# Kernel optimization log

Measured on AMD Instinct MI355X. Metric: run time of the kernel, lower is better.

## Reference

```python
import jax, jax.numpy as jnp
import numpy as np

N, G, E = 100000, 32768, 1000000
F, H = 64, 64


def _mlp(x, w1, b1, w2, b2):
    # Linear -> SiLU -> Linear (matches nn.Sequential in the torch module)
    return jax.nn.silu(x @ w1 + b1) @ w2 + b2


def setup_inputs() -> dict:
    key = jax.random.key(0)
    ks = jax.random.split(key, 24)

    def lin(k, fan_in, fan_out):
        s = 1.0 / np.sqrt(fan_in)
        kw, kb = jax.random.split(k)
        w = jax.random.uniform(kw, (fan_in, fan_out), jnp.float32, -s, s)
        b = jax.random.uniform(kb, (fan_out,), jnp.float32, -s, s)
        return w, b

    node_w1, node_b1 = lin(ks[0], F, H)
    node_w2, node_b2 = lin(ks[1], H, H)
    edge_w1, edge_b1 = lin(ks[2], 6, H)
    edge_w2, edge_b2 = lin(ks[3], H, H)
    msg_w1, msg_b1 = lin(ks[4], 2 * H, H)
    msg_w2, msg_b2 = lin(ks[5], H, H)
    upd_w1, upd_b1 = lin(ks[6], H, H)
    upd_w2, upd_b2 = lin(ks[7], H, H)

    return {
        "node_features": jax.random.normal(ks[8], (N, F), jnp.float32),
        "node_pos": jax.random.normal(ks[9], (N, 3), jnp.float32),
        "grid_pos": jax.random.normal(ks[10], (G, 3), jnp.float32),
        "orientations": jax.random.normal(ks[11], (N, 3, 3), jnp.float32),
        "edge_index": jnp.stack([
            jax.random.randint(ks[12], (E,), 0, N),
            jax.random.randint(ks[13], (E,), 0, G),
        ]),
        "node_w1": node_w1, "node_b1": node_b1, "node_w2": node_w2, "node_b2": node_b2,
        "edge_w1": edge_w1, "edge_b1": edge_b1, "edge_w2": edge_w2, "edge_b2": edge_b2,
        "msg_w1": msg_w1, "msg_b1": msg_b1, "msg_w2": msg_w2, "msg_b2": msg_b2,
        "upd_w1": upd_w1, "upd_b1": upd_b1, "upd_w2": upd_w2, "upd_b2": upd_b2,
    }


def reference(node_features, node_pos, grid_pos, orientations, edge_index,
              node_w1, node_b1, node_w2, node_b2,
              edge_w1, edge_b1, edge_w2, edge_b2,
              msg_w1, msg_b1, msg_w2, msg_b2,
              upd_w1, upd_b1, upd_w2, upd_b2):
    source, target = edge_index[0], edge_index[1]
    num_grid = grid_pos.shape[0]

    # node MLP
    h_node = _mlp(node_features, node_w1, node_b1, node_w2, node_b2)  # [N,H]

    # per-edge message with orientation-aware projection
    pos_s = node_pos[source]                 # [E,3]
    rel = grid_pos[target] - pos_s           # [E,3]
    # bmm(rel[:,None,:], R[source]).squeeze(1) == einsum ei,eij->ej
    trel = jnp.einsum("ei,eij->ej", rel, orientations[source])
    edge_attr = jnp.concatenate([pos_s, trel], axis=-1)        # [E,6]
    e_feat = _mlp(edge_attr, edge_w1, edge_b1, edge_w2, edge_b2)
    msg_in = jnp.concatenate([h_node[source], e_feat], axis=-1)  # [E,2H]
    messages = _mlp(msg_in, msg_w1, msg_b1, msg_w2, msg_b2)      # [E,H]

    # scatter-mean into grid buckets (mask out-of-range targets)
    valid = (target >= 0) & (target < num_grid)
    idx = jnp.where(valid, target, 0)
    msg_masked = jnp.where(valid[:, None], messages, 0.0)
    sums = jax.ops.segment_sum(msg_masked, idx, num_segments=num_grid)
    cnts = jax.ops.segment_sum(valid.astype(jnp.float32), idx, num_segments=num_grid)
    grid_feat = sums / jnp.maximum(cnts, 1.0)[:, None]

    return _mlp(grid_feat, upd_w1, upd_b1, upd_w2, upd_b2)  # [G,H]
```

## Files before the change

### kernel.cpp

```cpp
#include <hip/hip_runtime.h>
#include <cstdint>

typedef __attribute__((ext_vector_type(8))) short short8;
typedef __attribute__((ext_vector_type(4))) float f32x4;
typedef unsigned short u16;

__device__ __forceinline__ float b2f(u16 u) {
  union { unsigned int i; float f; } v; v.i = ((unsigned int)u) << 16; return v.f;
}
__device__ __forceinline__ u16 f2b(float f) {
  union { float f; unsigned int i; } v; v.f = f;
  unsigned int x = v.i;
  return (u16)((x + 0x7fffu + ((x >> 16) & 1u)) >> 16);
}
__device__ __forceinline__ float silu_f(float x) { return x / (1.0f + __expf(-x)); }

__device__ __forceinline__ float loadF(const void* p, long i, int isf32) {
  if (isf32) return ((const float*)p)[i];
  return b2f(((const u16*)p)[i]);
}

struct Ptrs { const void* p[20]; int n[20]; };

#define FW_NW1 0
#define FW_NW2 4096
#define FW_UW1 8192
#define FW_UW2 12288
#define FW_EW1 16384
#define FW_NB1 16768
#define FW_NB2 16832
#define FW_UB1 16896
#define FW_UB2 16960
#define FW_EB1 17024
#define FW_EB2 17088
#define FW_MB1 17152
#define FW_MB2 17216
#define FW_TOTAL 17280

#define IMG_EW2 0
#define IMG_MW1 4608
#define IMG_MW2 13312
#define IMG_TOTAL 17920

__global__ __launch_bounds__(256) void detect_k(Ptrs a, int* flags) {
  int j = blockIdx.x;
  const u16* q = (const u16*)a.p[j];
  int n = a.n[j];
  int m = n < 4096 ? n : 4096;
  int cnt = 0;
  for (int i = threadIdx.x; i < m; i += 256) {
    unsigned e = (q[i] >> 7) & 0xffu;
    if (e >= 0xC0u) cnt++;
  }
  __shared__ int tot;
  if (threadIdx.x == 0) tot = 0;
  __syncthreads();
  if (cnt) atomicAdd(&tot, cnt);
  __syncthreads();
  if (threadIdx.x == 0) flags[j] = (tot >= 2) ? 1 : 0;
}

__global__ __launch_bounds__(256) void prep_k(Ptrs a, const int* flags,
                                              u16* img, float* fw) {
  int i = blockIdx.x * 256 + threadIdx.x;
  if (i < IMG_TOTAL) {
    u16 val = 0;
    if (i < IMG_MW1) {
      int nn = i / 72, k = i % 72;
      if (k < 64) val = f2b(loadF(a.p[10], (long)k * 64 + nn, flags[10]));
    } else if (i < IMG_MW2) {
      int t2 = i - IMG_MW1; int nn = t2 / 136, k = t2 % 136;
      if (k < 128) val = f2b(loadF(a.p[12], (long)k * 64 + nn, flags[12]));
    } else {
      int t2 = i - IMG_MW2; int nn = t2 / 72, k = t2 % 72;
      if (k < 64) val = f2b(loadF(a.p[14], (long)k * 64 + nn, flags[14]));
    }
    img[i] = val;
  } else if (i < IMG_TOTAL + FW_TOTAL) {
    int j = i - IMG_TOTAL;
    float v;
    if (j < 4096)            v = loadF(a.p[4],  j,          flags[4]);
    else if (j < 8192)       v = loadF(a.p[6],  j - 4096,   flags[6]);
    else if (j < 12288)      v = loadF(a.p[16], j - 8192,   flags[16]);
    else if (j < 16384)      v = loadF(a.p[18], j - 12288,  flags[18]);
    else if (j < 16768)      v = loadF(a.p[8],  j - 16384,  flags[8]);
    else {
      int b = j - 16768; int seg = b >> 6, c = b & 63;
      const void* bp; int bf;
      switch (seg) {
        case 0: bp = a.p[5];  bf = flags[5];  break;
        case 1: bp = a.p[7];  bf = flags[7];  break;
        case 2: bp = a.p[17]; bf = flags[17]; break;
        case 3: bp = a.p[19]; bf = flags[19]; break;
        case 4: bp = a.p[9];  bf = flags[9];  break;
        case 5: bp = a.p[11]; bf = flags[11]; break;
        case 6: bp = a.p[13]; bf = flags[13]; break;
        default: bp = a.p[15]; bf = flags[15]; break;
      }
      v = loadF(bp, c, bf);
    }
    fw[j] = v;
  }
}

__global__ __launch_bounds__(256) void hist_k(const int* __restrict__ eidx,
                                              int* __restrict__ cnt, long E, int G) {
  long i = (long)blockIdx.x * 256 + threadIdx.x;
  const long stride = (long)gridDim.x * 256;
  for (; i < E; i += stride) {
    int tg = eidx[E + i];
    if (tg >= 0 && tg < G) atomicAdd(&cnt[tg], 1);
  }
}

__global__ __launch_bounds__(1024) void scan_k(const int* __restrict__ cnt,
                                               int* __restrict__ cursor,
                                               int* __restrict__ evp, int G) {
  __shared__ int sd[1024];
  __shared__ int carry;
  const int t = threadIdx.x;
  if (t == 0) carry = 0;
  __syncthreads();
  for (int c0 = 0; c0 < G; c0 += 1024) {
    int i = c0 + t;
    int v = (i < G) ? cnt[i] : 0;
    sd[t] = v;
    __syncthreads();
    for (int off = 1; off < 1024; off <<= 1) {
      int x = (t >= off) ? sd[t - off] : 0;
      __syncthreads();
      sd[t] += x;
      __syncthreads();
    }
    int excl = sd[t] - v + carry;
    if (i < G) cursor[i] = excl;
    int tot = sd[1023];
    __syncthreads();
    if (t == 0) carry += tot;
    __syncthreads();
  }
  if (t == 0) *evp = carry;
}

__global__ __launch_bounds__(256) void scat_k(const int* __restrict__ eidx,
                                              int* __restrict__ cursor,
                                              unsigned int* __restrict__ pkS,
                                              long E, int G) {
  long i = (long)blockIdx.x * 256 + threadIdx.x;
  const long stride = (long)gridDim.x * 256;
  for (; i < E; i += stride) {
    int tg = eidx[E + i];
    if (tg >= 0 && tg < G) {
      int s = eidx[i];
      int p = atomicAdd(&cursor[tg], 1);
      pkS[p] = (unsigned int)s | ((unsigned int)tg << 17);
    }
  }
}

__global__ __launch_bounds__(256) void node_mlp(
    const void* x, const int* flags, const float* fw, u16* out, int nrows)
{
  __shared__ float xs[64][68];
  __shared__ float w1s[64][68];
  __shared__ float w2s[64][68];
  __shared__ float b1s[64];
  __shared__ float b2s[64];
  const int t = threadIdx.x;
  const int xf = flags[0];
  const long rbase = (long)blockIdx.x * 64;
  for (int i = t; i < 4096; i += 256) {
    int k = i >> 6, cc = i & 63;
    w1s[k][cc] = fw[FW_NW1 + i];
    w2s[k][cc] = fw[FW_NW2 + i];
  }
  if (t < 64) { b1s[t] = fw[FW_NB1 + t]; b2s[t] = fw[FW_NB2 + t]; }
  {
    int row = t >> 2, ch = t & 3;
    long rg = rbase + row;
    if (rg < nrows) {
      if (xf) {
        const float* xp = (const float*)x + rg * 64 + ch * 16;
#pragma unroll
        for (int m = 0; m < 16; ++m) xs[row][ch * 16 + m] = xp[m];
      } else {
        const u16* xp = (const u16*)x + rg * 64 + ch * 16;
#pragma unroll
        for (int m = 0; m < 16; ++m) xs[row][ch * 16 + m] = b2f(xp[m]);
      }
    } else {
#pragma unroll
      for (int m = 0; m < 16; ++m) xs[row][ch * 16 + m] = 0.f;
    }
  }
  __syncthreads();
  const int r0 = (t >> 4) * 4, c0 = (t & 15) * 4;
  float acc[4][4];
#pragma unroll
  for (int i = 0; i < 4; ++i)
#pragma unroll
    for (int j = 0; j < 4; ++j) acc[i][j] = b1s[c0 + j];
  for (int k = 0; k < 64; ++k) {
    float w0 = w1s[k][c0], w1v = w1s[k][c0 + 1], w2v = w1s[k][c0 + 2], w3v = w1s[k][c0 + 3];
#pragma unroll
    for (int i = 0; i < 4; ++i) {
      float a = xs[r0 + i][k];
      acc[i][0] = fmaf(a, w0, acc[i][0]);
      acc[i][1] = fmaf(a, w1v, acc[i][1]);
      acc[i][2] = fmaf(a, w2v, acc[i][2]);
      acc[i][3] = fmaf(a, w3v, acc[i][3]);
    }
  }
  __syncthreads();
#pragma unroll
  for (int i = 0; i < 4; ++i)
#pragma unroll
    for (int j = 0; j < 4; ++j) xs[r0 + i][c0 + j] = silu_f(acc[i][j]);
  __syncthreads();
  float acc2[4][4];
#pragma unroll
  for (int i = 0; i < 4; ++i)
#pragma unroll
    for (int j = 0; j < 4; ++j) acc2[i][j] = b2s[c0 + j];
  for (int k = 0; k < 64; ++k) {
    float w0 = w2s[k][c0], w1v = w2s[k][c0 + 1], w2v = w2s[k][c0 + 2], w3v = w2s[k][c0 + 3];
#pragma unroll
    for (int i = 0; i < 4; ++i) {
      float a = xs[r0 + i][k];
      acc2[i][0] = fmaf(a, w0, acc2[i][0]);
      acc2[i][1] = fmaf(a, w1v, acc2[i][1]);
      acc2[i][2] = fmaf(a, w2v, acc2[i][2]);
      acc2[i][3] = fmaf(a, w3v, acc2[i][3]);
    }
  }
#pragma unroll
  for (int i = 0; i < 4; ++i) {
    long rg = rbase + r0 + i;
    if (rg < nrows) {
#pragma unroll
      for (int j = 0; j < 4; ++j) out[rg * 64 + c0 + j] = f2b(acc2[i][j]);
    }
  }
}

#define ETILES 4

__global__ __launch_bounds__(256, 3) void edge_kernel(
    const void* node_pos, const void* grid_pos, const void* orient,
    const unsigned int* __restrict__ pkS, const int* __restrict__ evp,
    const u16* __restrict__ h_node, const u16* __restrict__ img,
    const float* __restrict__ fw, const int* __restrict__ flags,
    float* __restrict__ sums, int G)
{
  __shared__ __align__(16) u16 hA[64][136];
  __shared__ __align__(16) u16 ef1[64][72];
  __shared__ __align__(16) float msgf[64][66];
  __shared__ float eaf[64][6];
  __shared__ float w1e[6][64];
  __shared__ float biasE[4][64];
  __shared__ int src_s[64];
  __shared__ int tgt_s[64];

  const int t = threadIdx.x;
  const int pf = flags[1], gf = flags[2], of = flags[3];
  const int Ev = *evp;

  for (int i = t; i < 384; i += 256) w1e[i / 64][i % 64] = fw[FW_EW1 + i];
  { int seg = t >> 6, cc = t & 63; biasE[seg][cc] = fw[FW_EB1 + seg * 64 + cc]; }

  const int lane = t & 63, w = t >> 6;
  const int q = lane >> 4, c = lane & 15;
  const int m0 = w * 16;
  const u16* wE2 = img + IMG_EW2;
  const u16* wM1 = img + IMG_MW1;
  const u16* wM2 = img + IMG_MW2;
  const f32x4 z = {0.f, 0.f, 0.f, 0.f};

  for (int tile = 0; tile < ETILES; ++tile) {
    long base = ((long)blockIdx.x * ETILES + tile) * 64;
    if (base >= Ev) break;
    __syncthreads();
    if (t < 64) {
      long eg = base + t;
      int s, tg;
      if (eg < Ev) {
        unsigned int pk = pkS[eg];
        s = (int)(pk & 0x1FFFFu);
        tg = (int)(pk >> 17);
      } else { s = 0; tg = -1; }
      src_s[t] = s;
      tgt_s[t] = tg;
      int tgc = (tg >= 0) ? tg : 0;
      float ps[3], rel[3], tr[3];
#pragma unroll
      for (int i = 0; i < 3; ++i) {
        ps[i] = loadF(node_pos, (long)s * 3 + i, pf);
        rel[i] = loadF(grid_pos, (long)tgc * 3 + i, gf) - ps[i];
      }
#pragma unroll
      for (int j = 0; j < 3; ++j) tr[j] = 0.f;
#pragma unroll
      for (int i = 0; i < 3; ++i)
#pragma unroll
        for (int j = 0; j < 3; ++j)
          tr[j] = fmaf(rel[i], loadF(orient, (long)s * 9 + i * 3 + j, of), tr[j]);
      eaf[t][0] = ps[0]; eaf[t][1] = ps[1]; eaf[t][2] = ps[2];
      eaf[t][3] = tr[0]; eaf[t][4] = tr[1]; eaf[t][5] = tr[2];
    }
    __syncthreads();
    {
      int e = t >> 2, ch = t & 3;
      const u16* hp = h_node + (long)src_s[e] * 64 + ch * 16;
      short8 v0 = *(const short8*)hp;
      short8 v1 = *(const short8*)(hp + 8);
      *(short8*)&hA[e][ch * 16] = v0;
      *(short8*)&hA[e][ch * 16 + 8] = v1;
    }
    __syncthreads();

    {
      int e = t >> 2, c0 = (t & 3) * 16;
      float a0 = eaf[e][0], a1 = eaf[e][1], a2 = eaf[e][2];
      float a3 = eaf[e][3], a4 = eaf[e][4], a5 = eaf[e][5];
      __align__(16) u16 tmp[16];
#pragma unroll
      for (int j = 0; j < 16; ++j) {
        int cc = c0 + j;
        float acc = biasE[0][cc];
        acc = fmaf(a0, w1e[0][cc], acc);
        acc = fmaf(a1, w1e[1][cc], acc);
        acc = fmaf(a2, w1e[2][cc], acc);
        acc = fmaf(a3, w1e[3][cc], acc);
        acc = fmaf(a4, w1e[4][cc], acc);
        acc = fmaf(a5, w1e[5][cc], acc);
        tmp[j] = f2b(silu_f(acc));
      }
      *(short8*)&ef1[e][c0] = *(const short8*)tmp;
      *(short8*)&ef1[e][c0 + 8] = *(const short8*)(tmp + 8);
    }
    __syncthreads();
    {
      short8 a0 = *(const short8*)&ef1[m0 + c][q * 8];
      short8 a1 = *(const short8*)&ef1[m0 + c][32 + q * 8];
#pragma unroll
      for (int nt = 0; nt < 4; ++nt) {
        short8 b0 = *(const short8*)&wE2[(nt * 16 + c) * 72 + q * 8];
        short8 b1v = *(const short8*)&wE2[(nt * 16 + c) * 72 + 32 + q * 8];
        f32x4 acc = __builtin_amdgcn_mfma_f32_16x16x32_bf16(a0, b0, z, 0, 0, 0);
        acc = __builtin_amdgcn_mfma_f32_16x16x32_bf16(a1, b1v, acc, 0, 0, 0);
#pragma unroll
        for (int r = 0; r < 4; ++r) {
          int row = m0 + q * 4 + r, col = nt * 16 + c;
          hA[row][64 + col] = f2b(acc[r] + biasE[1][col]);
        }
      }
    }
    __syncthreads();
    {
      short8 a0 = *(const short8*)&hA[m0 + c][q * 8];
      short8 a1 = *(const short8*)&hA[m0 + c][32 + q * 8];
      short8 a2 = *(const short8*)&hA[m0 + c][64 + q * 8];
      short8 a3 = *(const short8*)&hA[m0 + c][96 + q * 8];
#pragma unroll
      for (int nt = 0; nt < 4; ++nt) {
        const u16* wp = &wM1[(nt * 16 + c) * 136];
        f32x4 acc = __builtin_amdgcn_mfma_f32_16x16x32_bf16(a0, *(const short8*)(wp + q * 8), z, 0, 0, 0);
        acc = __builtin_amdgcn_mfma_f32_16x16x32_bf16(a1, *(const short8*)(wp + 32 + q * 8), acc, 0, 0, 0);
        acc = __builtin_amdgcn_mfma_f32_16x16x32_bf16(a2, *(const short8*)(wp + 64 + q * 8), acc, 0, 0, 0);
        acc = __builtin_amdgcn_mfma_f32_16x16x32_bf16(a3, *(const short8*)(wp + 96 + q * 8), acc, 0, 0, 0);
#pragma unroll
        for (int r = 0; r < 4; ++r) {
          int row = m0 + q * 4 + r, col = nt * 16 + c;
          ef1[row][col] = f2b(silu_f(acc[r] + biasE[2][col]));
        }
      }
    }
    __syncthreads();
    {
      short8 a0 = *(const short8*)&ef1[m0 + c][q * 8];
      short8 a1 = *(const short8*)&ef1[m0 + c][32 + q * 8];
#pragma unroll
      for (int nt = 0; nt < 4; ++nt) {
        short8 b0 = *(const short8*)&wM2[(nt * 16 + c) * 72 + q * 8];
        short8 b1v = *(const short8*)&wM2[(nt * 16 + c) * 72 + 32 + q * 8];
        f32x4 acc = __builtin_amdgcn_mfma_f32_16x16x32_bf16(a0, b0, z, 0, 0, 0);
        acc = __builtin_amdgcn_mfma_f32_16x16x32_bf16(a1, b1v, acc, 0, 0, 0);
#pragma unroll
        for (int r = 0; r < 4; ++r) {
          int row = m0 + q * 4 + r, col = nt * 16 + c;
          msgf[row][col] = acc[r] + biasE[3][col];
        }
      }
    }
    __syncthreads();
    {
      int col = lane;
      int r0 = w * 16;
      int cur = tgt_s[r0];
      float run = msgf[r0][col];
      bool lopen = (r0 == 0) ? true : (tgt_s[r0 - 1] == cur);
#pragma unroll
      for (int r2 = 1; r2 < 16; ++r2) {
        int r = r0 + r2;
        int tg = tgt_s[r];
        float v = msgf[r][col];
        if (tg == cur) {
          run += v;
        } else {
          if (cur >= 0) {
            if (lopen) unsafeAtomicAdd(&sums[(long)cur * 64 + col], run);
            else sums[(long)cur * 64 + col] = run;
          }
          cur = tg; run = v; lopen = false;
        }
      }
      bool ropen = (r0 + 16 >= 64) ? true : (tgt_s[r0 + 16] == cur);
      if (cur >= 0) {
        if (lopen || ropen) unsafeAtomicAdd(&sums[(long)cur * 64 + col], run);
        else sums[(long)cur * 64 + col] = run;
      }
    }
  }
}

__global__ __launch_bounds__(256) void upd_mlp(
    const float* __restrict__ sums, const int* __restrict__ cnt,
    const float* __restrict__ fw, float* __restrict__ out, int nrows)
{
  __shared__ float xs[64][68];
  __shared__ float w1s[64][68];
  __shared__ float w2s[64][68];
  __shared__ float b1s[64];
  __shared__ float b2s[64];
  const int t = threadIdx.x;
  const long rbase = (long)blockIdx.x * 64;
  for (int i = t; i < 4096; i += 256) {
    int k = i >> 6, cc = i & 63;
    w1s[k][cc] = fw[FW_UW1 + i];
    w2s[k][cc] = fw[FW_UW2 + i];
  }
  if (t < 64) { b1s[t] = fw[FW_UB1 + t]; b2s[t] = fw[FW_UB2 + t]; }
  {
    int row = t >> 2, ch = t & 3;
    long rg = rbase + row;
    if (rg < nrows) {
      float inv = 1.0f / fmaxf((float)cnt[rg], 1.0f);
      const float* p = sums + rg * 64 + ch * 16;
#pragma unroll
      for (int m = 0; m < 16; ++m) xs[row][ch * 16 + m] = p[m] * inv;
    } else {
#pragma unroll
      for (int m = 0; m < 16; ++m) xs[row][ch * 16 + m] = 0.f;
    }
  }
  __syncthreads();
  const int r0 = (t >> 4) * 4, c0 = (t & 15) * 4;
  float acc[4][4];
#pragma unroll
  for (int i = 0; i < 4; ++i)
#pragma unroll
    for (int j = 0; j < 4; ++j) acc[i][j] = b1s[c0 + j];
  for (int k = 0; k < 64; ++k) {
    float w0 = w1s[k][c0], w1v = w1s[k][c0 + 1], w2v = w1s[k][c0 + 2], w3v = w1s[k][c0 + 3];
#pragma unroll
    for (int i = 0; i < 4; ++i) {
      float a = xs[r0 + i][k];
      acc[i][0] = fmaf(a, w0, acc[i][0]);
      acc[i][1] = fmaf(a, w1v, acc[i][1]);
      acc[i][2] = fmaf(a, w2v, acc[i][2]);
      acc[i][3] = fmaf(a, w3v, acc[i][3]);
    }
  }
  __syncthreads();
#pragma unroll
  for (int i = 0; i < 4; ++i)
#pragma unroll
    for (int j = 0; j < 4; ++j) xs[r0 + i][c0 + j] = silu_f(acc[i][j]);
  __syncthreads();
  float acc2[4][4];
#pragma unroll
  for (int i = 0; i < 4; ++i)
#pragma unroll
    for (int j = 0; j < 4; ++j) acc2[i][j] = b2s[c0 + j];
  for (int k = 0; k < 64; ++k) {
    float w0 = w2s[k][c0], w1v = w2s[k][c0 + 1], w2v = w2s[k][c0 + 2], w3v = w2s[k][c0 + 3];
#pragma unroll
    for (int i = 0; i < 4; ++i) {
      float a = xs[r0 + i][k];
      acc2[i][0] = fmaf(a, w0, acc2[i][0]);
      acc2[i][1] = fmaf(a, w1v, acc2[i][1]);
      acc2[i][2] = fmaf(a, w2v, acc2[i][2]);
      acc2[i][3] = fmaf(a, w3v, acc2[i][3]);
    }
  }
#pragma unroll
  for (int i = 0; i < 4; ++i) {
    long rg = rbase + r0 + i;
    if (rg < nrows) {
#pragma unroll
      for (int j = 0; j < 4; ++j) out[rg * 64 + c0 + j] = acc2[i][j];
    }
  }
}

extern "C" void kernel_launch(void* const* d_in, const int* in_sizes, int n_in,
                              void* d_out, int out_size, void* d_ws, size_t ws_size,
                              hipStream_t stream) {
  const int N = in_sizes[1] / 3;
  const int G = in_sizes[2] / 3;
  const long E = (long)in_sizes[4] / 2;

  char* ws = (char*)d_ws;
  int* flags = (int*)ws;
  int* evp = flags + 24;
  float* sums = (float*)(ws + 256);
  size_t off = 256 + (size_t)G * 256;
  int* cnt = (int*)(ws + off);     off += (size_t)G * 4;
  int* cursor = (int*)(ws + off);  off += (size_t)G * 4;
  unsigned int* pkS = (unsigned int*)(ws + off); off += (size_t)E * 4;
  u16* h_node = (u16*)(ws + off);  off += (size_t)N * 128;
  u16* img = (u16*)(ws + off);     off += (size_t)IMG_TOTAL * 2;
  float* fw = (float*)(ws + off);

  hipMemsetAsync(ws, 0, 256 + (size_t)G * 256 + (size_t)G * 4, stream);

  Ptrs a;
  const int map[20] = {0,1,2,3, 5,6,7,8, 9,10,11,12, 13,14,15,16, 17,18,19,20};
  for (int i = 0; i < 20; ++i) { a.p[i] = d_in[map[i]]; a.n[i] = in_sizes[map[i]]; }

  detect_k<<<20, 256, 0, stream>>>(a, flags);
  prep_k<<<(IMG_TOTAL + FW_TOTAL + 255) / 256, 256, 0, stream>>>(a, flags, img, fw);
  hist_k<<<1024, 256, 0, stream>>>((const int*)d_in[4], cnt, E, G);
  scan_k<<<1, 1024, 0, stream>>>(cnt, cursor, evp, G);
  node_mlp<<<(N + 63) / 64, 256, 0, stream>>>(d_in[0], flags, fw, h_node, N);
  scat_k<<<1024, 256, 0, stream>>>((const int*)d_in[4], cursor, pkS, E, G);
  edge_kernel<<<(int)((E + ETILES * 64 - 1) / (ETILES * 64)), 256, 0, stream>>>(
      d_in[1], d_in[2], d_in[3], pkS, evp, h_node, img, fw, flags,
      sums, G);
  upd_mlp<<<(G + 63) / 64, 256, 0, stream>>>(sums, cnt, fw, (float*)d_out, G);
}
```

Baseline: 529.3 us.

## Parallelize prefix scan across blocks and alias msg buffer to raise edge occupancy

Replaces the single-block sequential scan over all grid buckets with a multi-block per-chunk scan plus a tiny serial block-offset pass, and has the scatter kernel add the block offset. Separately, the edge kernel reuses the hA shared buffer for msgf and raises its launch bound from 3 to 5 blocks per CU, cutting LDS footprint to allow more resident blocks. The aliasing is only safe if hA is no longer needed once msgf is written, and the tighter launch bound may force register spills.

```diff
diff --git a/kernel.cpp b/kernel.cpp
--- a/kernel.cpp
+++ b/kernel.cpp
@@ -113,37 +113,37 @@
   }
 }
 
-__global__ __launch_bounds__(1024) void scan_k(const int* __restrict__ cnt,
-                                               int* __restrict__ cursor,
-                                               int* __restrict__ evp, int G) {
+__global__ __launch_bounds__(1024) void scan1_k(const int* __restrict__ cnt,
+                                                int* __restrict__ cursor,
+                                                int* __restrict__ bsum, int G) {
   __shared__ int sd[1024];
-  __shared__ int carry;
   const int t = threadIdx.x;
-  if (t == 0) carry = 0;
-  __syncthreads();
-  for (int c0 = 0; c0 < G; c0 += 1024) {
-    int i = c0 + t;
-    int v = (i < G) ? cnt[i] : 0;
-    sd[t] = v;
-    __syncthreads();
-    for (int off = 1; off < 1024; off <<= 1) {
-      int x = (t >= off) ? sd[t - off] : 0;
-      __syncthreads();
-      sd[t] += x;
-      __syncthreads();
-    }
-    int excl = sd[t] - v + carry;
-    if (i < G) cursor[i] = excl;
-    int tot = sd[1023];
-    __syncthreads();
-    if (t == 0) carry += tot;
-    __syncthreads();
-  }
-  if (t == 0) *evp = carry;
+  int i = blockIdx.x * 1024 + t;
+  int v = (i < G) ? cnt[i] : 0;
+  sd[t] = v;
+  __syncthreads();
+  for (int off = 1; off < 1024; off <<= 1) {
+    int x = (t >= off) ? sd[t - off] : 0;
+    __syncthreads();
+    sd[t] += x;
+    __syncthreads();
+  }
+  if (i < G) cursor[i] = sd[t] - v;
+  if (t == 1023) bsum[blockIdx.x] = sd[t];
+}
+
+__global__ void scan2_k(const int* __restrict__ bsum, int* __restrict__ boffs,
+                        int* __restrict__ evp, int nb) {
+  if (threadIdx.x == 0 && blockIdx.x == 0) {
+    int acc = 0;
+    for (int i = 0; i < nb; ++i) { boffs[i] = acc; acc += bsum[i]; }
+    *evp = acc;
+  }
 }
 
 __global__ __launch_bounds__(256) void scat_k(const int* __restrict__ eidx,
                                               int* __restrict__ cursor,
+                                              const int* __restrict__ boffs,
                                               unsigned int* __restrict__ pkS,
                                               long E, int G) {
   long i = (long)blockIdx.x * 256 + threadIdx.x;
@@ -152,7 +152,7 @@
     int tg = eidx[E + i];
     if (tg >= 0 && tg < G) {
       int s = eidx[i];
-      int p = atomicAdd(&cursor[tg], 1);
+      int p = atomicAdd(&cursor[tg], 1) + boffs[tg >> 10];
       pkS[p] = (unsigned int)s | ((unsigned int)tg << 17);
     }
   }
@@ -245,7 +245,7 @@
 
 #define ETILES 4
 
-__global__ __launch_bounds__(256, 3) void edge_kernel(
+__global__ __launch_bounds__(256, 5) void edge_kernel(
     const void* node_pos, const void* grid_pos, const void* orient,
     const unsigned int* __restrict__ pkS, const int* __restrict__ evp,
     const u16* __restrict__ h_node, const u16* __restrict__ img,
@@ -254,12 +254,12 @@
 {
   __shared__ __align__(16) u16 hA[64][136];
   __shared__ __align__(16) u16 ef1[64][72];
-  __shared__ __align__(16) float msgf[64][66];
   __shared__ float eaf[64][6];
   __shared__ float w1e[6][64];
   __shared__ float biasE[4][64];
   __shared__ int src_s[64];
   __shared__ int tgt_s[64];
+  float (*msgf)[66] = (float (*)[66])&hA[0][0];
 
   const int t = threadIdx.x;
   const int pf = flags[1], gf = flags[2], of = flags[3];
@@ -509,6 +509,7 @@
   const int N = in_sizes[1] / 3;
   const int G = in_sizes[2] / 3;
   const long E = (long)in_sizes[4] / 2;
+  const int NB = (G + 1023) / 1024;
 
   char* ws = (char*)d_ws;
   int* flags = (int*)ws;
@@ -517,6 +518,9 @@
   size_t off = 256 + (size_t)G * 256;
   int* cnt = (int*)(ws + off);     off += (size_t)G * 4;
   int* cursor = (int*)(ws + off);  off += (size_t)G * 4;
+  int* bsum = (int*)(ws + off);    off += (size_t)NB * 4;
+  int* boffs = (int*)(ws + off);   off += (size_t)NB * 4;
+  off = (off + 255) & ~(size_t)255;
   unsigned int* pkS = (unsigned int*)(ws + off); off += (size_t)E * 4;
   u16* h_node = (u16*)(ws + off);  off += (size_t)N * 128;
   u16* img = (u16*)(ws + off);     off += (size_t)IMG_TOTAL * 2;
@@ -531,9 +535,10 @@
   detect_k<<<20, 256, 0, stream>>>(a, flags);
   prep_k<<<(IMG_TOTAL + FW_TOTAL + 255) / 256, 256, 0, stream>>>(a, flags, img, fw);
   hist_k<<<1024, 256, 0, stream>>>((const int*)d_in[4], cnt, E, G);
-  scan_k<<<1, 1024, 0, stream>>>(cnt, cursor, evp, G);
+  scan1_k<<<NB, 1024, 0, stream>>>(cnt, cursor, bsum, G);
+  scan2_k<<<1, 64, 0, stream>>>(bsum, boffs, evp, NB);
   node_mlp<<<(N + 63) / 64, 256, 0, stream>>>(d_in[0], flags, fw, h_node, N);
-  scat_k<<<1024, 256, 0, stream>>>((const int*)d_in[4], cursor, pkS, E, G);
+  scat_k<<<1024, 256, 0, stream>>>((const int*)d_in[4], cursor, boffs, pkS, E, G);
   edge_kernel<<<(int)((E + ETILES * 64 - 1) / (ETILES * 64)), 256, 0, stream>>>(
       d_in[1], d_in[2], d_in[3], pkS, evp, h_node, img, fw, flags,
       sums, G);
```

New measurement: 468.9 us. 11.4% less time.
